# Kernel optimization log

Measured on AMD Instinct MI355X. Metric: run time of the kernel, lower is better.

Reference implementation:

```python
import jax, jax.numpy as jnp
import numpy as np

H = 256; HID = 128; V = 50000; LV = 200
N = 512; L = 64; M = 64; C = 4; T = 8; K = 8; E = 2048


def _gru_cell(x, h, wih, whh, bih, bhh):
    gi = x @ wih.T + bih
    gh = h @ whh.T + bhh
    ir, iz, inn = jnp.split(gi, 3, -1)
    hr, hz, hn = jnp.split(gh, 3, -1)
    r = jax.nn.sigmoid(ir + hr)
    z = jax.nn.sigmoid(iz + hz)
    n = jnp.tanh(inn + r * hn)
    return (1.0 - z) * n + z * h


def _bigru(x, wih, whh, bih, bhh):
    # x: [B, L, D]; params stacked [2, ...] = (fwd, bwd). out [B, L, 2*hid]
    B = x.shape[0]
    hid = whh.shape[-1]
    def run(xseq, d):
        def step(h, xt):
            hn = _gru_cell(xt, h, wih[d], whh[d], bih[d], bhh[d])
            return hn, hn
        _, out = jax.lax.scan(step, jnp.zeros((B, hid), x.dtype), jnp.swapaxes(xseq, 0, 1))
        return jnp.swapaxes(out, 0, 1)
    fwd = run(x, 0)
    bwd = jnp.flip(run(jnp.flip(x, 1), 1), 1)
    return jnp.concatenate([fwd, bwd], -1)


def _attn_pool(x, w, b):
    # x: [..., L, H]; softmax over L (matches torch softmax(dim=0) per sequence)
    a = jnp.einsum('...lh,h->...l', x, w) + b
    wts = jax.nn.softmax(a, axis=-1)
    return jnp.einsum('...l,...lh->...h', wts, x)


def _forward(seq_emb, seq_wih, seq_whh, seq_bih, seq_bhh, seq_pw, seq_pb,
             ctx_wih, ctx_whh, ctx_bih, ctx_bhh, ctx_pw, ctx_pb,
             ast_label_tab, ast_tok_tab, ast_pw, ast_pb,
             tl_wiou, tl_biou, tl_uiou, tl_wf, tl_bf, tl_uf,
             fa_wih, fa_whh, fa_bih, fa_bhh, fa_aw, fa_ab,
             comb_w, comb_b, g1_w, g1_b, g2_w, g2_b,
             cls_w1, cls_b1, cls_w2, cls_b2,
             seq_tokens, ast_children, ast_child_mask, ast_label_ids, ast_tok_ids, ctx_nei, edges):
    n_stmt = seq_tokens.shape[1]
    # --- three sequence encoders (stmt/varname/vartype), vmapped over encoder axis
    def enc(toks, emb, wih, whh, bih, bhh, pw, pb):
        e = emb[toks]                              # [N, L, H]
        o = _bigru(e, wih, whh, bih, bhh)          # [N, L, H]
        return _attn_pool(o, pw, pb)               # [N, H]
    vecs = jax.vmap(enc)(seq_tokens, seq_emb, seq_wih, seq_whh, seq_bih, seq_bhh, seq_pw, seq_pb)
    stmt_v, varn_v, vart_v = vecs[0], vecs[1], vecs[2]
    # --- ChildSum TreeLSTM over AST, batched over statements, scanned by node index
    # (children always have lower index than parent -> valid topological order)
    tok_e = ast_tok_tab[ast_tok_ids].mean(2)       # [N, M, H]
    xn = 0.5 * ast_label_tab[ast_label_ids] + 0.5 * tok_e
    Mn = xn.shape[1]
    xs = jnp.swapaxes(xn, 0, 1)                    # [M, N, H]
    chs = jnp.swapaxes(ast_children, 0, 1)         # [M, N, C]
    cms = jnp.swapaxes(ast_child_mask, 0, 1).astype(xn.dtype)
    nidx = jnp.arange(xn.shape[0])[:, None]
    def tl_step(carry, inp):
        h_arr, c_arr = carry                       # [M, N, H] each
        m, x, ch, msk = inp
        ch_h = h_arr[ch, nidx] * msk[..., None]    # [N, C, H], masked children
        ch_c = c_arr[ch, nidx] * msk[..., None]
        h_sum = ch_h.sum(1)
        iou = x @ tl_wiou.T + tl_biou + h_sum @ tl_uiou.T
        i, o, u = jnp.split(iou, 3, -1)
        i = jax.nn.sigmoid(i); o = jax.nn.sigmoid(o); u = jnp.tanh(u)
        fg = jax.nn.sigmoid((x @ tl_wf.T + tl_bf)[:, None, :] + ch_h @ tl_uf.T)
        c = i * u + (fg * ch_c).sum(1)
        h = o * jnp.tanh(c)
        return (h_arr.at[m].set(h), c_arr.at[m].set(c)), None
    z0 = jnp.zeros((Mn, xn.shape[0], xn.shape[2]), xn.dtype)
    (h_arr, _), _ = jax.lax.scan(tl_step, (z0, z0), (jnp.arange(Mn), xs, chs, cms))
    ast_v = _attn_pool(jnp.swapaxes(h_arr, 0, 1), ast_pw, ast_pb)   # [N, H]
    # --- context encoder over neighbor statement vectors (detached in original)
    ctx_in = jax.lax.stop_gradient(stmt_v)[ctx_nei]                 # [N, K, H]
    ctx_v = _attn_pool(_bigru(ctx_in, ctx_wih, ctx_whh, ctx_bih, ctx_bhh), ctx_pw, ctx_pb)
    # --- feature attention over the 5 per-statement feature vectors
    feats = jnp.stack([stmt_v, ast_v, varn_v, vart_v, ctx_v], axis=1)  # [N, 5, H]
    o = _bigru(feats, fa_wih, fa_whh, fa_bih, fa_bhh)
    wts = jax.nn.softmax(o @ fa_aw + fa_ab, axis=-1)
    x = jnp.einsum('nl,nlh->nh', wts, feats)
    # --- neighbor-mean combine (undirected unique edges)
    e0, e1 = edges[:, 0], edges[:, 1]
    rows = jnp.concatenate([e0, e1]); srcs = jnp.concatenate([e1, e0])
    nei_sum = jax.ops.segment_sum(x[srcs], rows, num_segments=n_stmt)
    deg = jax.ops.segment_sum(jnp.ones(rows.shape[0], x.dtype), rows, num_segments=n_stmt)
    nei_mean = nei_sum / jnp.maximum(deg, 1.0)[:, None]
    x2 = jax.nn.relu(jnp.concatenate([x, nei_mean], -1) @ comb_w.T + comb_b)
    # --- 2-layer symmetric-normalized GCN (edges both directions + self loops)
    sl = jnp.arange(n_stmt)
    r2 = jnp.concatenate([e0, e1, sl]); c2 = jnp.concatenate([e1, e0, sl])
    d2 = jax.ops.segment_sum(jnp.ones(r2.shape[0], x.dtype), r2, num_segments=n_stmt)
    dis = jnp.maximum(d2, 1.0) ** -0.5
    norm = (dis[r2] * dis[c2])[:, None]
    spmm = lambda y: jax.ops.segment_sum(norm * y[c2], r2, num_segments=n_stmt)
    h1 = jax.nn.relu(spmm(x2 @ g1_w.T + g1_b))
    h2 = jax.nn.relu(spmm(h1 @ g2_w.T + g2_b))
    gvec = jnp.concatenate([h2.mean(0), h2.max(0)], -1)
    return (jax.nn.relu(gvec @ cls_w1.T + cls_b1) @ cls_w2.T + cls_b2)[0]


def setup_inputs() -> dict:
    rng = np.random.default_rng(0)
    ks = iter(jax.random.split(jax.random.key(0), 64))
    def p(shape, s=0.05):
        return jax.random.normal(next(ks), shape, dtype=jnp.float32) * s
    inp = {}
    inp['seq_tokens'] = jnp.asarray(rng.integers(0, V, (3, N, L)), jnp.int32)
    ub = np.maximum(np.arange(M), 1)
    inp['ast_children'] = jnp.asarray((rng.random((N, M, C)) * ub[None, :, None]).astype(np.int64), jnp.int32)
    inp['ast_child_mask'] = jnp.asarray((rng.random((N, M, C)) < 0.7) & (np.arange(M)[None, :, None] > 0))
    inp['ast_label_ids'] = jnp.asarray(rng.integers(0, LV, (N, M)), jnp.int32)
    inp['ast_tok_ids'] = jnp.asarray(rng.integers(0, V, (N, M, T)), jnp.int32)
    inp['ctx_nei'] = jnp.asarray(rng.integers(0, N, (N, K)), jnp.int32)
    pairs = rng.integers(0, N, (8 * E, 2))
    pairs = pairs[pairs[:, 0] < pairs[:, 1]]
    pairs = np.unique(pairs, axis=0)[:E]
    inp['edges'] = jnp.asarray(pairs, jnp.int32)
    inp['seq_emb'] = p((3, V, H)).at[:, 0].set(0.0)  # padding_idx=0
    inp['seq_wih'] = p((3, 2, 3 * HID, H)); inp['seq_whh'] = p((3, 2, 3 * HID, HID))
    inp['seq_bih'] = p((3, 2, 3 * HID)); inp['seq_bhh'] = p((3, 2, 3 * HID))
    inp['seq_pw'] = p((3, H)); inp['seq_pb'] = p((3,))
    inp['ctx_wih'] = p((2, 3 * HID, H)); inp['ctx_whh'] = p((2, 3 * HID, HID))
    inp['ctx_bih'] = p((2, 3 * HID)); inp['ctx_bhh'] = p((2, 3 * HID))
    inp['ctx_pw'] = p((H,)); inp['ctx_pb'] = p(())
    inp['ast_label_tab'] = p((LV, H)); inp['ast_tok_tab'] = p((V, H))
    inp['ast_pw'] = p((H,)); inp['ast_pb'] = p(())
    inp['tl_wiou'] = p((3 * H, H)); inp['tl_biou'] = p((3 * H,)); inp['tl_uiou'] = p((3 * H, H))
    inp['tl_wf'] = p((H, H)); inp['tl_bf'] = p((H,)); inp['tl_uf'] = p((H, H))
    inp['fa_wih'] = p((2, 3 * HID, H)); inp['fa_whh'] = p((2, 3 * HID, HID))
    inp['fa_bih'] = p((2, 3 * HID)); inp['fa_bhh'] = p((2, 3 * HID))
    inp['fa_aw'] = p((H,)); inp['fa_ab'] = p(())
    inp['comb_w'] = p((H, 2 * H)); inp['comb_b'] = p((H,))
    inp['g1_w'] = p((H, H)); inp['g1_b'] = p((H,))
    inp['g2_w'] = p((H, H)); inp['g2_b'] = p((H,))
    inp['cls_w1'] = p((H, 2 * H)); inp['cls_b1'] = p((H,))
    inp['cls_w2'] = p((1, H)); inp['cls_b2'] = p((1,))
    return inp


def reference(seq_emb, seq_wih, seq_whh, seq_bih, seq_bhh, seq_pw, seq_pb,
              ctx_wih, ctx_whh, ctx_bih, ctx_bhh, ctx_pw, ctx_pb,
              ast_label_tab, ast_tok_tab, ast_pw, ast_pb,
              tl_wiou, tl_biou, tl_uiou, tl_wf, tl_bf, tl_uf,
              fa_wih, fa_whh, fa_bih, fa_bhh, fa_aw, fa_ab,
              comb_w, comb_b, g1_w, g1_b, g2_w, g2_b,
              cls_w1, cls_b1, cls_w2, cls_b2,
              seq_tokens, ast_children, ast_child_mask, ast_label_ids, ast_tok_ids, ctx_nei, edges):
    return _forward(seq_emb, seq_wih, seq_whh, seq_bih, seq_bhh, seq_pw, seq_pb,
                    ctx_wih, ctx_whh, ctx_bih, ctx_bhh, ctx_pw, ctx_pb,
                    ast_label_tab, ast_tok_tab, ast_pw, ast_pb,
                    tl_wiou, tl_biou, tl_uiou, tl_wf, tl_bf, tl_uf,
                    fa_wih, fa_whh, fa_bih, fa_bhh, fa_aw, fa_ab,
                    comb_w, comb_b, g1_w, g1_b, g2_w, g2_b,
                    cls_w1, cls_b1, cls_w2, cls_b2,
                    seq_tokens, ast_children, ast_child_mask, ast_label_ids, ast_tok_ids, ctx_nei, edges)
```

## Files before the change

### kernel.cpp

```cpp
#include <hip/hip_runtime.h>
#include <hip/hip_bf16.h>
#include <cmath>


__device__ __forceinline__ float sigf(float x) { return 1.f / (1.f + expf(-x)); }
__device__ __forceinline__ float b2f(__hip_bfloat16 x) { return __bfloat162float(x); }

typedef __attribute__((ext_vector_type(8))) short bf16x8v;
typedef __attribute__((ext_vector_type(4))) float f32x4;

__device__ __forceinline__ void gload16(const __hip_bfloat16* g, __hip_bfloat16* l) {
  __builtin_amdgcn_global_load_lds((const __attribute__((address_space(1))) void*)g,
                                   (__attribute__((address_space(3))) void*)l, 16, 0, 0);
}

__global__ __launch_bounds__(256) void k_build_wx(const float* __restrict__ wiou,
                                                  const float* __restrict__ wf,
                                                  const float* __restrict__ biou,
                                                  const float* __restrict__ bf,
                                                  float* __restrict__ w,
                                                  float* __restrict__ b) {
  int i = blockIdx.x * 256 + threadIdx.x;
  if (i < 1024 * 256) {
    int j = i >> 8, k = i & 255;
    w[i] = (j < 768) ? wiou[j * 256 + k] : wf[(j - 768) * 256 + k];
  }
  if (i < 1024) b[i] = (i < 768) ? biou[i] : bf[i - 768];
}

__global__ __launch_bounds__(256) void k_build_wproj(const float* __restrict__ uiou,
                                                     const float* __restrict__ uf,
                                                     float* __restrict__ w) {
  int i = blockIdx.x * 256 + threadIdx.x;
  if (i >= 1024 * 256) return;
  int j = i >> 8, k = i & 255;
  w[i] = (j < 768) ? uiou[j * 256 + k] : uf[(j - 768) * 256 + k];
}

__global__ __launch_bounds__(256) void k_zero_misc(float* __restrict__ nei_sum,
                                                   int* __restrict__ deg,
                                                   int* __restrict__ flag) {
  int i = blockIdx.x * 256 + threadIdx.x;
  if (i < 512 * 256) nei_sum[i] = 0.f;
  if (i < 512) deg[i] = 0;
  if (i == 0) *flag = 0;
}

__global__ __launch_bounds__(256) void k_mask_detect(const unsigned* __restrict__ raw,
                                                     int* __restrict__ flag) {
  int i = blockIdx.x * 256 + threadIdx.x;
  if (i < 32768) {
    if (raw[i] > 1u) atomicOr(flag, 1);
  }
}

__global__ __launch_bounds__(256) void k_mask_convert(const void* __restrict__ raw,
                                                      const int* __restrict__ flag,
                                                      int* __restrict__ msk) {
  int i = blockIdx.x * 256 + threadIdx.x;
  if (i >= 512 * 64 * 4) return;
  int v;
  if (*flag) v = ((const unsigned char*)raw)[i] != 0;
  else       v = ((const int*)raw)[i] != 0;
  msk[i] = v;
}

__global__ __launch_bounds__(256) void k_cvt_bf16(const float* __restrict__ A,
                                                  const int* __restrict__ ridx,
                                                  int rstride,
                                                  __hip_bfloat16* __restrict__ out) {
  int r = blockIdx.x * 8 + (threadIdx.x >> 5);
  int k = (threadIdx.x & 31) * 8;
  const float* src = A + (size_t)(ridx ? ridx[r] : r) * rstride + k;
  float4 v0 = *(const float4*)src;
  float4 v1 = *(const float4*)(src + 4);
  union { ushort4 u; __hip_bfloat16 b[4]; } p0, p1;
  p0.b[0] = __float2bfloat16(v0.x); p0.b[1] = __float2bfloat16(v0.y);
  p0.b[2] = __float2bfloat16(v0.z); p0.b[3] = __float2bfloat16(v0.w);
  p1.b[0] = __float2bfloat16(v1.x); p1.b[1] = __float2bfloat16(v1.y);
  p1.b[2] = __float2bfloat16(v1.z); p1.b[3] = __float2bfloat16(v1.w);
  __hip_bfloat16* dst = out + (size_t)r * 256 + k;
  *(ushort4*)dst = p0.u;
  *(ushort4*)(dst + 4) = p1.u;
}

__global__ __launch_bounds__(256) void k_gemm_mfma(const __hip_bfloat16* __restrict__ A,
                                                   const __hip_bfloat16* __restrict__ W,
                                                   const float* __restrict__ bias,
                                                   void* __restrict__ Cv,
                                                   int R, int K, int J,
                                                   int relu, int out_bf16) {
  __shared__ __align__(16) __hip_bfloat16 As[128 * 32];
  __shared__ __align__(16) __hip_bfloat16 Bs[128 * 32];
  int njt = J >> 7;
  int rt = blockIdx.x / njt;
  int jt = blockIdx.x - rt * njt;
  int tid = threadIdx.x;
  int w = tid >> 6, lane = tid & 63;
  int wr = w >> 1, wc = w & 1;

  const __hip_bfloat16* ga = A + (size_t)(rt * 128 + w * 32 + (lane >> 2)) * K + (lane & 3) * 8;
  const __hip_bfloat16* gb = W + (size_t)(jt * 128 + w * 32 + (lane >> 2)) * K + (lane & 3) * 8;
  __hip_bfloat16* lA0 = As + w * 1024;
  __hip_bfloat16* lB0 = Bs + w * 1024;
  size_t gstep16 = (size_t)16 * K;

  f32x4 acc[4][4];
#pragma unroll
  for (int m = 0; m < 4; ++m)
#pragma unroll
    for (int n = 0; n < 4; ++n) acc[m][n] = (f32x4){0.f, 0.f, 0.f, 0.f};

  int fr = lane & 15;
  int kg = (lane >> 4) * 8;
  const __hip_bfloat16* raA = As + (size_t)(wr * 64 + fr) * 32 + kg;
  const __hip_bfloat16* raB = Bs + (size_t)(wc * 64 + fr) * 32 + kg;

  for (int k0 = 0; k0 < K; k0 += 32) {
    __syncthreads();
    gload16(ga, lA0);
    gload16(ga + gstep16, lA0 + 512);
    gload16(gb, lB0);
    gload16(gb + gstep16, lB0 + 512);
    ga += 32; gb += 32;
    __syncthreads();
    bf16x8v a[4], b[4];
#pragma unroll
    for (int m = 0; m < 4; ++m) a[m] = *(const bf16x8v*)(raA + m * 512);
#pragma unroll
    for (int n = 0; n < 4; ++n) b[n] = *(const bf16x8v*)(raB + n * 512);
#pragma unroll
    for (int m = 0; m < 4; ++m)
#pragma unroll
      for (int n = 0; n < 4; ++n)
        acc[m][n] = __builtin_amdgcn_mfma_f32_16x16x32_bf16(a[m], b[n], acc[m][n], 0, 0, 0);
  }

  int row0 = rt * 128 + wr * 64 + (lane >> 4) * 4;
  int col0 = jt * 128 + wc * 64 + fr;
#pragma unroll
  for (int n = 0; n < 4; ++n) {
    int col = col0 + n * 16;
    float bv = bias ? bias[col] : 0.f;
#pragma unroll
    for (int m = 0; m < 4; ++m) {
#pragma unroll
      for (int j = 0; j < 4; ++j) {
        float v = acc[m][n][j] + bv;
        if (relu) v = fmaxf(v, 0.f);
        size_t idx = (size_t)(row0 + m * 16 + j) * J + col;
        if (out_bf16) ((__hip_bfloat16*)Cv)[idx] = __float2bfloat16(v);
        else ((float*)Cv)[idx] = v;
      }
    }
  }
}

__global__ __launch_bounds__(256) void k_gemm128(const float* __restrict__ A,
                                                 const int* __restrict__ ridx,
                                                 int rstride,
                                                 const float* __restrict__ W,
                                                 const float* __restrict__ bias,
                                                 float* __restrict__ C,
                                                 int R, int K, int J, int relu,
                                                 int out_bf16) {
  __shared__ float As[16][132];
  __shared__ float Ws[16][132];
  int njt = J >> 7;
  int rt = blockIdx.x / njt;
  int jt = blockIdx.x % njt;
  int tid = threadIdx.x;
  int tx = tid & 15, ty = tid >> 4;

  int row2 = tid >> 1;
  int kq = (tid & 1) * 4;
  int gr = rt * 128 + row2;
  const float* arow = A + (size_t)(ridx ? ridx[gr] : gr) * rstride;
  const float* wrow = W + (size_t)(jt * 128 + row2) * K;

  float acc[8][8];
#pragma unroll
  for (int i = 0; i < 8; ++i)
#pragma unroll
    for (int j = 0; j < 8; ++j) acc[i][j] = 0.f;

  for (int k0 = 0; k0 < K; k0 += 16) {
    float4 av0 = *(const float4*)(arow + k0 + kq);
    float4 av1 = *(const float4*)(arow + k0 + kq + 8);
    float4 wv0 = *(const float4*)(wrow + k0 + kq);
    float4 wv1 = *(const float4*)(wrow + k0 + kq + 8);
    __syncthreads();
    As[kq + 0][row2] = av0.x; As[kq + 1][row2] = av0.y;
    As[kq + 2][row2] = av0.z; As[kq + 3][row2] = av0.w;
    As[kq + 8][row2] = av1.x; As[kq + 9][row2] = av1.y;
    As[kq + 10][row2] = av1.z; As[kq + 11][row2] = av1.w;
    Ws[kq + 0][row2] = wv0.x; Ws[kq + 1][row2] = wv0.y;
    Ws[kq + 2][row2] = wv0.z; Ws[kq + 3][row2] = wv0.w;
    Ws[kq + 8][row2] = wv1.x; Ws[kq + 9][row2] = wv1.y;
    Ws[kq + 10][row2] = wv1.z; Ws[kq + 11][row2] = wv1.w;
    __syncthreads();
#pragma unroll
    for (int kk = 0; kk < 16; ++kk) {
      float a[8], b[8];
      *(float4*)&a[0] = *(const float4*)&As[kk][ty * 4];
      *(float4*)&a[4] = *(const float4*)&As[kk][64 + ty * 4];
      *(float4*)&b[0] = *(const float4*)&Ws[kk][tx * 4];
      *(float4*)&b[4] = *(const float4*)&Ws[kk][64 + tx * 4];
#pragma unroll
      for (int i = 0; i < 8; ++i)
#pragma unroll
        for (int j = 0; j < 8; ++j) acc[i][j] += a[i] * b[j];
    }
  }

  int col0 = jt * 128 + tx * 4;
  int col1 = jt * 128 + 64 + tx * 4;
  float b0[4], b1[4];
#pragma unroll
  for (int j = 0; j < 4; ++j) {
    b0[j] = bias ? bias[col0 + j] : 0.f;
    b1[j] = bias ? bias[col1 + j] : 0.f;
  }
#pragma unroll
  for (int i = 0; i < 8; ++i) {
    int row = rt * 128 + ((i < 4) ? (ty * 4 + i) : (64 + ty * 4 + i - 4));
    float v0[4], v1[4];
#pragma unroll
    for (int j = 0; j < 4; ++j) {
      float x0 = acc[i][j] + b0[j];
      float x1 = acc[i][j + 4] + b1[j];
      if (relu) { x0 = fmaxf(x0, 0.f); x1 = fmaxf(x1, 0.f); }
      v0[j] = x0; v1[j] = x1;
    }
    if (out_bf16) {
      __hip_bfloat16* Cb = (__hip_bfloat16*)C;
      union { ushort4 u; __hip_bfloat16 b[4]; } p0, p1;
#pragma unroll
      for (int j = 0; j < 4; ++j) { p0.b[j] = __float2bfloat16(v0[j]); p1.b[j] = __float2bfloat16(v1[j]); }
      *(ushort4*)(Cb + (size_t)row * J + col0) = p0.u;
      *(ushort4*)(Cb + (size_t)row * J + col1) = p1.u;
    } else {
      *(float4*)(C + (size_t)row * J + col0) = *(float4*)v0;
      *(float4*)(C + (size_t)row * J + col1) = *(float4*)v1;
    }
  }
}

__global__ __launch_bounds__(512, 2) void k_gru3(const __hip_bfloat16* __restrict__ gi,
                                                 const float* __restrict__ whh,
                                                 const float* __restrict__ bhh,
                                                 float* __restrict__ out,
                                                 int L) {
  __shared__ float hs[4][132];
  __shared__ float parts[4][8][388];
  int tid = threadIdx.x;
  int d = blockIdx.y;
  int n0 = blockIdx.x * 4;
  int ks = tid >> 6;
  int rg = tid & 63;
  int kb = ks * 16;
  const float* wbase = whh + (size_t)d * 384 * 128;

  float4 w4[6][4];
#pragma unroll
  for (int r = 0; r < 6; ++r) {
    const float* wr = wbase + (size_t)(r * 64 + rg) * 128 + kb;
#pragma unroll
    for (int q = 0; q < 4; ++q) w4[r][q] = ((const float4*)wr)[q];
  }

  int sg = tid >> 7, jg = tid & 127;
  const float* bh = bhh + d * 384;
  float br = bh[jg], bz = bh[128 + jg], bn = bh[256 + jg];

  for (int i = tid; i < 4 * 132; i += 512) ((float*)hs)[i] = 0.f;
  __syncthreads();

  int t = d ? (L - 1) : 0;
  int dt = d ? -1 : 1;

  for (int step = 0; step < L; ++step, t += dt) {
    const __hip_bfloat16* g = gi + (size_t)((n0 + sg) * L + t) * 768 + d * 384;
    float pgr = b2f(g[jg]), pgz = b2f(g[128 + jg]), pgn = b2f(g[256 + jg]);

    float acc[4][6];
#pragma unroll
    for (int s = 0; s < 4; ++s)
#pragma unroll
      for (int r = 0; r < 6; ++r) acc[s][r] = 0.f;
#pragma unroll
    for (int s = 0; s < 4; ++s) {
#pragma unroll
      for (int q = 0; q < 4; ++q) {
        float4 hv = *(const float4*)&hs[s][kb + q * 4];
#pragma unroll
        for (int r = 0; r < 6; ++r) {
          acc[s][r] += w4[r][q].x * hv.x + w4[r][q].y * hv.y +
                       w4[r][q].z * hv.z + w4[r][q].w * hv.w;
        }
      }
    }
#pragma unroll
    for (int s = 0; s < 4; ++s)
#pragma unroll
      for (int r = 0; r < 6; ++r) parts[s][ks][r * 64 + rg] = acc[s][r];
    __syncthreads();
    {
      float sr = 0.f, sz = 0.f, sn = 0.f;
#pragma unroll
      for (int k = 0; k < 8; ++k) {
        sr += parts[sg][k][jg];
        sz += parts[sg][k][128 + jg];
        sn += parts[sg][k][256 + jg];
      }
      float r = sigf(pgr + sr + br);
      float z = sigf(pgz + sz + bz);
      float nn = tanhf(pgn + r * (sn + bn));
      float hold = hs[sg][jg];
      float hnew = (1.f - z) * nn + z * hold;
      hs[sg][jg] = hnew;
      out[(size_t)((n0 + sg) * L + t) * 256 + d * 128 + jg] = hnew;
    }
    __syncthreads();
  }
}

__global__ __launch_bounds__(256) void k_attn_pool(const float* __restrict__ score_src,
                                                   int s_ns, int s_ls,
                                                   const float* __restrict__ val_src,
                                                   int v_ns, int v_ls,
                                                   const float* __restrict__ w,
                                                   const float* __restrict__ bptr,
                                                   float* __restrict__ dst,
                                                   int dst_stride, int L) {
  __shared__ float wts[64];
  int n = blockIdx.x;
  int tid = threadIdx.x;
  if (tid < 64) {
    float a = -INFINITY;
    if (tid < L) {
      const float* row = score_src + (size_t)n * s_ns + (size_t)tid * s_ls;
      float s = bptr[0];
      for (int h = 0; h < 256; h += 4) {
        float4 v = *(const float4*)(row + h);
        float4 wv = *(const float4*)(w + h);
        s += v.x * wv.x + v.y * wv.y + v.z * wv.z + v.w * wv.w;
      }
      a = s;
    }
    float mx = a;
#pragma unroll
    for (int off = 32; off; off >>= 1) mx = fmaxf(mx, __shfl_xor(mx, off));
    float e = (tid < L) ? expf(a - mx) : 0.f;
    float ss = e;
#pragma unroll
    for (int off = 32; off; off >>= 1) ss += __shfl_xor(ss, off);
    if (tid < L) wts[tid] = e / ss;
  }
  __syncthreads();
  float acc = 0.f;
  for (int l = 0; l < L; ++l)
    acc += wts[l] * val_src[(size_t)n * v_ns + (size_t)l * v_ls + tid];
  dst[(size_t)n * dst_stride + tid] = acc;
}

__global__ __launch_bounds__(256) void k_xn_bf16(const float* __restrict__ label_tab,
                                                 const float* __restrict__ tok_tab,
                                                 const int* __restrict__ lbl_ids,
                                                 const int* __restrict__ tok_ids,
                                                 __hip_bfloat16* __restrict__ xnb) {
  int nm = blockIdx.x;
  int h = threadIdx.x;
  const int* tids = tok_ids + (size_t)nm * 8;
  float s = 0.f;
#pragma unroll
  for (int t = 0; t < 8; ++t) s += tok_tab[(size_t)tids[t] * 256 + h];
  float v = 0.5f * label_tab[(size_t)lbl_ids[nm] * 256 + h] + 0.0625f * s;
  xnb[(size_t)nm * 256 + h] = __float2bfloat16(v);
}

__global__ __launch_bounds__(256) void k_tl_combine4(const __hip_bfloat16* __restrict__ HU,
                                                     const __hip_bfloat16* __restrict__ XWALL,
                                                     const int* __restrict__ ch,
                                                     const int* __restrict__ msk,
                                                     float* __restrict__ h_arr,
                                                     float* __restrict__ c_arr,
                                                     __hip_bfloat16* __restrict__ hbf,
                                                     int m) {
  int n = blockIdx.x, h = threadIdx.x;
  const __hip_bfloat16* xw = XWALL + ((size_t)(n * 64 + m)) * 1024;
  float si = b2f(xw[h]), so = b2f(xw[256 + h]), su = b2f(xw[512 + h]);
  float xfv = b2f(xw[768 + h]);
  const int* chp = ch + ((size_t)(n * 64 + m)) * 4;
  const int* mkp = msk + ((size_t)(n * 64 + m)) * 4;
  float cs = 0.f;
#pragma unroll
  for (int c = 0; c < 4; ++c) {
    if (mkp[c]) {
      int cc = chp[c];
      const __hip_bfloat16* hu = HU + ((size_t)cc * 512 + n) * 1024;
      si += b2f(hu[h]);
      so += b2f(hu[256 + h]);
      su += b2f(hu[512 + h]);
      float fg = sigf(xfv + b2f(hu[768 + h]));
      cs += fg * c_arr[((size_t)cc * 512 + n) * 256 + h];
    }
  }
  float iv = sigf(si), ov = sigf(so), uv = tanhf(su);
  float cn = iv * uv + cs;
  float hn = ov * tanhf(cn);
  h_arr[((size_t)m * 512 + n) * 256 + h] = hn;
  c_arr[((size_t)m * 512 + n) * 256 + h] = cn;
  hbf[(size_t)n * 256 + h] = __float2bfloat16(hn);
}

__global__ __launch_bounds__(256) void k_edge_deg(const int* __restrict__ edges,
                                                  int* __restrict__ deg, int E) {
  int i = blockIdx.x * 256 + threadIdx.x;
  if (i < E) {
    atomicAdd(&deg[edges[2 * i]], 1);
    atomicAdd(&deg[edges[2 * i + 1]], 1);
  }
}

__global__ __launch_bounds__(256) void k_nei(const int* __restrict__ edges,
                                             const float* __restrict__ x,
                                             float* __restrict__ nei_sum) {
  int e = blockIdx.x, h = threadIdx.x;
  int a = edges[2 * e], b = edges[2 * e + 1];
  atomicAdd(&nei_sum[(size_t)a * 256 + h], x[(size_t)b * 256 + h]);
  atomicAdd(&nei_sum[(size_t)b * 256 + h], x[(size_t)a * 256 + h]);
}

__global__ __launch_bounds__(256) void k_xcat(const float* __restrict__ x,
                                              const float* __restrict__ nei_sum,
                                              const int* __restrict__ deg,
                                              float* __restrict__ xcat) {
  int n = blockIdx.x, h = threadIdx.x;
  xcat[(size_t)n * 512 + h] = x[(size_t)n * 256 + h];
  float d = fmaxf((float)deg[n], 1.f);
  xcat[(size_t)n * 512 + 256 + h] = nei_sum[(size_t)n * 256 + h] / d;
}

__global__ __launch_bounds__(256) void k_spmm_self(const float* __restrict__ y,
                                                   const int* __restrict__ deg,
                                                   float* __restrict__ ob) {
  int n = blockIdx.x, h = threadIdx.x;
  float dis2 = 1.f / (float)(deg[n] + 1);
  ob[(size_t)n * 256 + h] = dis2 * y[(size_t)n * 256 + h];
}

__global__ __launch_bounds__(256) void k_spmm_edge(const float* __restrict__ y,
                                                   const int* __restrict__ deg,
                                                   const int* __restrict__ edges,
                                                   float* __restrict__ ob) {
  int e = blockIdx.x, h = threadIdx.x;
  int a = edges[2 * e], b = edges[2 * e + 1];
  float w = (1.f / sqrtf((float)(deg[a] + 1))) * (1.f / sqrtf((float)(deg[b] + 1)));
  atomicAdd(&ob[(size_t)a * 256 + h], w * y[(size_t)b * 256 + h]);
  atomicAdd(&ob[(size_t)b * 256 + h], w * y[(size_t)a * 256 + h]);
}

__global__ __launch_bounds__(256) void k_relu_inplace(float* __restrict__ p) {
  int i = blockIdx.x * 256 + threadIdx.x;
  p[i] = fmaxf(p[i], 0.f);
}

__global__ __launch_bounds__(256) void k_final(const float* __restrict__ h2,
                                               const float* __restrict__ w1,
                                               const float* __restrict__ b1,
                                               const float* __restrict__ w2,
                                               const float* __restrict__ b2,
                                               float* __restrict__ outp) {
  __shared__ float gv[512];
  __shared__ float zz[256];
  int tid = threadIdx.x;
  float mn = 0.f, mx = -INFINITY;
  for (int n = 0; n < 512; ++n) {
    float v = h2[(size_t)n * 256 + tid];
    mn += v;
    mx = fmaxf(mx, v);
  }
  gv[tid] = mn / 512.f;
  gv[256 + tid] = mx;
  __syncthreads();
  float acc = b1[tid];
  for (int k = 0; k < 512; ++k) acc += gv[k] * w1[(size_t)tid * 512 + k];
  zz[tid] = fmaxf(acc, 0.f) * w2[tid];
  __syncthreads();
  for (int s = 128; s; s >>= 1) {
    if (tid < s) zz[tid] += zz[tid + s];
    __syncthreads();
  }
  if (tid == 0) outp[0] = zz[0] + b2[0];
}

extern "C" void kernel_launch(void* const* d_in, const int* in_sizes, int n_in,
                              void* d_out, int out_size, void* d_ws, size_t ws_size,
                              hipStream_t stream) {
  const int* seq_tokens    = (const int*)d_in[0];
  const int* ast_children  = (const int*)d_in[1];
  const void* ast_mask_raw = (const void*)d_in[2];
  const int* ast_label_ids = (const int*)d_in[3];
  const int* ast_tok_ids   = (const int*)d_in[4];
  const int* ctx_nei       = (const int*)d_in[5];
  const int* edges         = (const int*)d_in[6];
  const float* seq_emb  = (const float*)d_in[7];
  const float* seq_wih  = (const float*)d_in[8];
  const float* seq_whh  = (const float*)d_in[9];
  const float* seq_bih  = (const float*)d_in[10];
  const float* seq_bhh  = (const float*)d_in[11];
  const float* seq_pw   = (const float*)d_in[12];
  const float* seq_pb   = (const float*)d_in[13];
  const float* ctx_wih  = (const float*)d_in[14];
  const float* ctx_whh  = (const float*)d_in[15];
  const float* ctx_bih  = (const float*)d_in[16];
  const float* ctx_bhh  = (const float*)d_in[17];
  const float* ctx_pw   = (const float*)d_in[18];
  const float* ctx_pb   = (const float*)d_in[19];
  const float* ast_label_tab = (const float*)d_in[20];
  const float* ast_tok_tab   = (const float*)d_in[21];
  const float* ast_pw   = (const float*)d_in[22];
  const float* ast_pb   = (const float*)d_in[23];
  const float* tl_wiou  = (const float*)d_in[24];
  const float* tl_biou  = (const float*)d_in[25];
  const float* tl_uiou  = (const float*)d_in[26];
  const float* tl_wf    = (const float*)d_in[27];
  const float* tl_bf    = (const float*)d_in[28];
  const float* tl_uf    = (const float*)d_in[29];
  const float* fa_wih   = (const float*)d_in[30];
  const float* fa_whh   = (const float*)d_in[31];
  const float* fa_bih   = (const float*)d_in[32];
  const float* fa_bhh   = (const float*)d_in[33];
  const float* fa_aw    = (const float*)d_in[34];
  const float* fa_ab    = (const float*)d_in[35];
  const float* comb_w   = (const float*)d_in[36];
  const float* comb_b   = (const float*)d_in[37];
  const float* g1_w     = (const float*)d_in[38];
  const float* g1_b     = (const float*)d_in[39];
  const float* g2_w     = (const float*)d_in[40];
  const float* g2_b     = (const float*)d_in[41];
  const float* cls_w1   = (const float*)d_in[42];
  const float* cls_b1   = (const float*)d_in[43];
  const float* cls_w2   = (const float*)d_in[44];
  const float* cls_b2   = (const float*)d_in[45];
  float* outp = (float*)d_out;
  float* ws = (float*)d_ws;
  int E = in_sizes[6] / 2;

  size_t off = 0;
  auto take = [&](size_t n) { size_t o = off; off += n; return o; };
  const size_t F_FEATS = take(512 * 5 * 256);
  const size_t F_X     = take(512 * 256);
  const size_t F_X2    = take(512 * 256);
  const size_t F_Y     = take(512 * 256);
  const size_t F_H1    = take(512 * 256);
  const size_t F_H2    = take(512 * 256);
  const size_t F_XCAT  = take(512 * 512);
  const size_t F_NEI   = take(512 * 256);
  const size_t F_DEG   = take(512);
  const size_t F_FLAG  = take(16);
  const size_t F_MSK   = take(512 * 64 * 4);
  const size_t F_WXW   = take(1024 * 256);
  const size_t F_WXB   = take(1024);
  const size_t F_WPROJ = take(1024 * 256);
  const size_t F_REGION = take(83886080);
  (void)ws_size;

  float* FEATS = ws + F_FEATS;
  float* X     = ws + F_X;
  float* X2    = ws + F_X2;
  float* Y     = ws + F_Y;
  float* H1    = ws + F_H1;
  float* H2    = ws + F_H2;
  float* XCAT  = ws + F_XCAT;
  float* NEI   = ws + F_NEI;
  int*   DEG   = (int*)(ws + F_DEG);
  int*   FLAG  = (int*)(ws + F_FLAG);
  int*   MSK   = (int*)(ws + F_MSK);
  float* WXW   = ws + F_WXW;
  float* WXB   = ws + F_WXB;
  float* WPROJ = ws + F_WPROJ;
  float* REG   = ws + F_REGION;
  __hip_bfloat16* GI16  = (__hip_bfloat16*)REG;
  float* OUT   = REG + 13631488;
  __hip_bfloat16* XWALL16 = (__hip_bfloat16*)REG;
  float* HARR  = REG + 17000000;
  float* CARR  = REG + 25500000;
  __hip_bfloat16* HU16 = (__hip_bfloat16*)(REG + 34000000);
  __hip_bfloat16* GIFA16 = (__hip_bfloat16*)REG;
  float* OUTFA = REG + 1966080;
  __hip_bfloat16* ABF     = (__hip_bfloat16*)(REG + 60000000);
  __hip_bfloat16* WSEQBF  = (__hip_bfloat16*)(REG + 65000000);
  __hip_bfloat16* WCTXBF  = (__hip_bfloat16*)(REG + 65400000);
  __hip_bfloat16* WFABF   = (__hip_bfloat16*)(REG + 65600000);
  __hip_bfloat16* WXWBF   = (__hip_bfloat16*)(REG + 65800000);
  __hip_bfloat16* WPROJBF = (__hip_bfloat16*)(REG + 66100000);
  __hip_bfloat16* HBF     = (__hip_bfloat16*)(REG + 66500000);

  auto gemm = [&](const float* A, const int* ridx, int rstride, const float* W,
                  const float* bias, float* C, int R, int K, int J, int relu,
                  int obf) {
    dim3 g((R / 128) * (J / 128));
    k_gemm128<<<g, 256, 0, stream>>>(A, ridx, rstride, W, bias, C, R, K, J, relu, obf);
  };
  auto cvt = [&](const float* A, const int* ridx, int rstride,
                 __hip_bfloat16* ob, int R) {
    k_cvt_bf16<<<R / 8, 256, 0, stream>>>(A, ridx, rstride, ob);
  };
  auto mgemm = [&](const __hip_bfloat16* A, const __hip_bfloat16* W,
                   const float* bias, void* C, int R, int K, int J, int relu,
                   int obf) {
    dim3 g((R / 128) * (J / 128));
    k_gemm_mfma<<<g, 256, 0, stream>>>(A, W, bias, C, R, K, J, relu, obf);
  };

  k_build_wx<<<1024, 256, 0, stream>>>(tl_wiou, tl_wf, tl_biou, tl_bf, WXW, WXB);
  k_build_wproj<<<1024, 256, 0, stream>>>(tl_uiou, tl_uf, WPROJ);
  k_zero_misc<<<512, 256, 0, stream>>>(NEI, DEG, FLAG);
  k_mask_detect<<<128, 256, 0, stream>>>((const unsigned*)ast_mask_raw, FLAG);
  k_mask_convert<<<512, 256, 0, stream>>>(ast_mask_raw, FLAG, MSK);
  cvt(seq_wih, nullptr, 256, WSEQBF, 2304);
  cvt(ctx_wih, nullptr, 256, WCTXBF, 768);
  cvt(fa_wih, nullptr, 256, WFABF, 768);
  cvt(WXW, nullptr, 256, WXWBF, 1024);
  cvt(WPROJ, nullptr, 256, WPROJBF, 1024);

  const int slot_of[3] = {0, 2, 3};
  for (int e = 0; e < 3; ++e) {
    cvt(seq_emb + (size_t)e * 50000 * 256, seq_tokens + (size_t)e * 32768, 256,
        ABF, 32768);
    mgemm(ABF, WSEQBF + (size_t)e * 768 * 256, seq_bih + (size_t)e * 768,
          GI16, 32768, 256, 768, 0, 1);
    k_gru3<<<dim3(128, 2), 512, 0, stream>>>(GI16, seq_whh + (size_t)e * 2 * 384 * 128,
                                             seq_bhh + (size_t)e * 768, OUT, 64);
    k_attn_pool<<<512, 256, 0, stream>>>(OUT, 64 * 256, 256, OUT, 64 * 256, 256,
                                         seq_pw + e * 256, seq_pb + e,
                                         FEATS + slot_of[e] * 256, 1280, 64);
  }

  cvt(FEATS, ctx_nei, 1280, ABF, 4096);
  mgemm(ABF, WCTXBF, ctx_bih, GI16, 4096, 256, 768, 0, 1);
  k_gru3<<<dim3(128, 2), 512, 0, stream>>>(GI16, ctx_whh, ctx_bhh, OUT, 8);
  k_attn_pool<<<512, 256, 0, stream>>>(OUT, 8 * 256, 256, OUT, 8 * 256, 256,
                                       ctx_pw, ctx_pb, FEATS + 4 * 256, 1280, 8);

  k_xn_bf16<<<32768, 256, 0, stream>>>(ast_label_tab, ast_tok_tab, ast_label_ids,
                                       ast_tok_ids, ABF);
  mgemm(ABF, WXWBF, WXB, XWALL16, 32768, 256, 1024, 0, 1);
  for (int m = 0; m < 64; ++m) {
    k_tl_combine4<<<512, 256, 0, stream>>>(HU16, XWALL16, ast_children, MSK,
                                           HARR, CARR, HBF, m);
    if (m < 63)
      mgemm(HBF, WPROJBF, nullptr, HU16 + (size_t)m * 512 * 1024,
            512, 256, 1024, 0, 1);
  }
  k_attn_pool<<<512, 256, 0, stream>>>(HARR, 256, 512 * 256, HARR, 256, 512 * 256,
                                       ast_pw, ast_pb, FEATS + 1 * 256, 1280, 64);

  cvt(FEATS, nullptr, 256, ABF, 2560);
  mgemm(ABF, WFABF, fa_bih, GIFA16, 2560, 256, 768, 0, 1);
  k_gru3<<<dim3(128, 2), 512, 0, stream>>>(GIFA16, fa_whh, fa_bhh, OUTFA, 5);
  k_attn_pool<<<512, 256, 0, stream>>>(OUTFA, 5 * 256, 256, FEATS, 1280, 256,
                                       fa_aw, fa_ab, X, 256, 5);

  k_edge_deg<<<(E + 255) / 256, 256, 0, stream>>>(edges, DEG, E);
  k_nei<<<E, 256, 0, stream>>>(edges, X, NEI);
  k_xcat<<<512, 256, 0, stream>>>(X, NEI, DEG, XCAT);
  gemm(XCAT, nullptr, 512, comb_w, comb_b, X2, 512, 512, 256, 1, 0);
  gemm(X2, nullptr, 256, g1_w, g1_b, Y, 512, 256, 256, 0, 0);
  k_spmm_self<<<512, 256, 0, stream>>>(Y, DEG, H1);
  k_spmm_edge<<<E, 256, 0, stream>>>(Y, DEG, edges, H1);
  k_relu_inplace<<<512, 256, 0, stream>>>(H1);
  gemm(H1, nullptr, 256, g2_w, g2_b, Y, 512, 256, 256, 0, 0);
  k_spmm_self<<<512, 256, 0, stream>>>(Y, DEG, H2);
  k_spmm_edge<<<E, 256, 0, stream>>>(Y, DEG, edges, H2);
  k_relu_inplace<<<512, 256, 0, stream>>>(H2);
  k_final<<<1, 256, 0, stream>>>(H2, cls_w1, cls_b1, cls_w2, cls_b2, outp);
}
```

Before: 2.200 ms.

## Rewrite GRU recurrence with bf16 MFMA over 16 sequences per block

Replaces the scalar-FMA GRU recurrence, which used register-held fp32 weights, 4 sequences per block and an 8-way LDS partial-sum reduction, with a kernel that issues 16x16x32 bf16 MFMA instructions over 16 sequences per block. The recurrent weights are pre-converted to bf16 and the hidden state is kept in LDS as bf16, with the gate math done 4 columns per thread. This removes the cross-warp reduction and the bulk of the scalar multiply-adds, but launches 4x fewer blocks (64 instead of 256), which may leave much of the GPU idle. It also adds bf16 rounding of the hidden state and weights on every step of the recurrence.

New measurement: 2.101 ms. 1.05x faster.

```diff
diff --git a/kernel.cpp b/kernel.cpp
--- a/kernel.cpp
+++ b/kernel.cpp
@@ -5,6 +5,9 @@
 
 __device__ __forceinline__ float sigf(float x) { return 1.f / (1.f + expf(-x)); }
 __device__ __forceinline__ float b2f(__hip_bfloat16 x) { return __bfloat162float(x); }
+__device__ __forceinline__ float bu2f(unsigned short u) {
+  union { float f; unsigned i; } v; v.i = ((unsigned)u) << 16; return v.f;
+}
 
 typedef __attribute__((ext_vector_type(8))) short bf16x8v;
 typedef __attribute__((ext_vector_type(4))) float f32x4;
@@ -246,81 +249,93 @@
   }
 }
 
-__global__ __launch_bounds__(512, 2) void k_gru3(const __hip_bfloat16* __restrict__ gi,
-                                                 const float* __restrict__ whh,
-                                                 const float* __restrict__ bhh,
-                                                 float* __restrict__ out,
-                                                 int L) {
-  __shared__ float hs[4][132];
-  __shared__ float parts[4][8][388];
+__global__ __launch_bounds__(512) void k_gru4(const __hip_bfloat16* __restrict__ gi,
+                                              const __hip_bfloat16* __restrict__ whhb,
+                                              const float* __restrict__ bhh,
+                                              float* __restrict__ out,
+                                              int L) {
+  __shared__ __align__(16) __hip_bfloat16 hsb[16][136];
+  __shared__ float outl[16][392];
   int tid = threadIdx.x;
   int d = blockIdx.y;
-  int n0 = blockIdx.x * 4;
-  int ks = tid >> 6;
-  int rg = tid & 63;
-  int kb = ks * 16;
-  const float* wbase = whh + (size_t)d * 384 * 128;
-
-  float4 w4[6][4];
-#pragma unroll
-  for (int r = 0; r < 6; ++r) {
-    const float* wr = wbase + (size_t)(r * 64 + rg) * 128 + kb;
-#pragma unroll
-    for (int q = 0; q < 4; ++q) w4[r][q] = ((const float4*)wr)[q];
-  }
-
-  int sg = tid >> 7, jg = tid & 127;
+  int n0 = blockIdx.x * 16;
+  int w = tid >> 6, lane = tid & 63;
+  int fr = lane & 15;
+  int kg = (lane >> 4) * 8;
+  int jw = w * 48;
+
+  bf16x8v bfr[3][4];
+  const __hip_bfloat16* wb = whhb + (size_t)d * 384 * 128;
+#pragma unroll
+  for (int cf = 0; cf < 3; ++cf)
+#pragma unroll
+    for (int kf = 0; kf < 4; ++kf)
+      bfr[cf][kf] = *(const bf16x8v*)(wb + (size_t)(jw + cf * 16 + fr) * 128 + kf * 32 + kg);
+
+  int s = tid >> 5;
+  int j0 = (tid & 31) * 4;
   const float* bh = bhh + d * 384;
-  float br = bh[jg], bz = bh[128 + jg], bn = bh[256 + jg];
-
-  for (int i = tid; i < 4 * 132; i += 512) ((float*)hs)[i] = 0.f;
+  float4 br = *(const float4*)(bh + j0);
+  float4 bz = *(const float4*)(bh + 128 + j0);
+  float4 bn = *(const float4*)(bh + 256 + j0);
+
+  float h[4] = {0.f, 0.f, 0.f, 0.f};
+  for (int i = tid; i < 16 * 136; i += 512) ((__hip_bfloat16*)hsb)[i] = __float2bfloat16(0.f);
   __syncthreads();
 
   int t = d ? (L - 1) : 0;
   int dt = d ? -1 : 1;
 
   for (int step = 0; step < L; ++step, t += dt) {
-    const __hip_bfloat16* g = gi + (size_t)((n0 + sg) * L + t) * 768 + d * 384;
-    float pgr = b2f(g[jg]), pgz = b2f(g[128 + jg]), pgn = b2f(g[256 + jg]);
-
-    float acc[4][6];
-#pragma unroll
-    for (int s = 0; s < 4; ++s)
-#pragma unroll
-      for (int r = 0; r < 6; ++r) acc[s][r] = 0.f;
-#pragma unroll
-    for (int s = 0; s < 4; ++s) {
-#pragma unroll
-      for (int q = 0; q < 4; ++q) {
-        float4 hv = *(const float4*)&hs[s][kb + q * 4];
-#pragma unroll
-        for (int r = 0; r < 6; ++r) {
-          acc[s][r] += w4[r][q].x * hv.x + w4[r][q].y * hv.y +
-                       w4[r][q].z * hv.z + w4[r][q].w * hv.w;
-        }
-      }
-    }
-#pragma unroll
-    for (int s = 0; s < 4; ++s)
-#pragma unroll
-      for (int r = 0; r < 6; ++r) parts[s][ks][r * 64 + rg] = acc[s][r];
+    const __hip_bfloat16* g = gi + (size_t)((n0 + s) * L + t) * 768 + d * 384 + j0;
+    ushort4 gr4 = *(const ushort4*)(g);
+    ushort4 gz4 = *(const ushort4*)(g + 128);
+    ushort4 gn4 = *(const ushort4*)(g + 256);
+
+    f32x4 acc[3];
+#pragma unroll
+    for (int cf = 0; cf < 3; ++cf) acc[cf] = (f32x4){0.f, 0.f, 0.f, 0.f};
+#pragma unroll
+    for (int kf = 0; kf < 4; ++kf) {
+      bf16x8v a = *(const bf16x8v*)(&hsb[fr][kf * 32 + kg]);
+#pragma unroll
+      for (int cf = 0; cf < 3; ++cf)
+        acc[cf] = __builtin_amdgcn_mfma_f32_16x16x32_bf16(a, bfr[cf][kf], acc[cf], 0, 0, 0);
+    }
+    int r0 = (lane >> 4) * 4;
+#pragma unroll
+    for (int cf = 0; cf < 3; ++cf) {
+      int col = jw + cf * 16 + fr;
+#pragma unroll
+      for (int r = 0; r < 4; ++r) outl[r0 + r][col] = acc[cf][r];
+    }
     __syncthreads();
-    {
-      float sr = 0.f, sz = 0.f, sn = 0.f;
-#pragma unroll
-      for (int k = 0; k < 8; ++k) {
-        sr += parts[sg][k][jg];
-        sz += parts[sg][k][128 + jg];
-        sn += parts[sg][k][256 + jg];
-      }
-      float r = sigf(pgr + sr + br);
-      float z = sigf(pgz + sz + bz);
-      float nn = tanhf(pgn + r * (sn + bn));
-      float hold = hs[sg][jg];
-      float hnew = (1.f - z) * nn + z * hold;
-      hs[sg][jg] = hnew;
-      out[(size_t)((n0 + sg) * L + t) * 256 + d * 128 + jg] = hnew;
-    }
+
+    float4 sr = *(const float4*)&outl[s][j0];
+    float4 sz = *(const float4*)&outl[s][128 + j0];
+    float4 sn = *(const float4*)&outl[s][256 + j0];
+    float gr[4] = {bu2f(gr4.x), bu2f(gr4.y), bu2f(gr4.z), bu2f(gr4.w)};
+    float gz[4] = {bu2f(gz4.x), bu2f(gz4.y), bu2f(gz4.z), bu2f(gz4.w)};
+    float gn[4] = {bu2f(gn4.x), bu2f(gn4.y), bu2f(gn4.z), bu2f(gn4.w)};
+    float srv[4] = {sr.x, sr.y, sr.z, sr.w};
+    float szv[4] = {sz.x, sz.y, sz.z, sz.w};
+    float snv[4] = {sn.x, sn.y, sn.z, sn.w};
+    float brv[4] = {br.x, br.y, br.z, br.w};
+    float bzv[4] = {bz.x, bz.y, bz.z, bz.w};
+    float bnv[4] = {bn.x, bn.y, bn.z, bn.w};
+#pragma unroll
+    for (int j = 0; j < 4; ++j) {
+      float r = sigf(gr[j] + srv[j] + brv[j]);
+      float z = sigf(gz[j] + szv[j] + bzv[j]);
+      float nn = tanhf(gn[j] + r * (snv[j] + bnv[j]));
+      h[j] = (1.f - z) * nn + z * h[j];
+    }
+    *(float4*)(out + (size_t)((n0 + s) * L + t) * 256 + d * 128 + j0) =
+        (float4){h[0], h[1], h[2], h[3]};
+    union { ushort4 u; __hip_bfloat16 b[4]; } hp;
+#pragma unroll
+    for (int j = 0; j < 4; ++j) hp.b[j] = __float2bfloat16(h[j]);
+    *(ushort4*)&hsb[s][j0] = hp.u;
     __syncthreads();
   }
 }
@@ -597,6 +612,9 @@
   __hip_bfloat16* WXWBF   = (__hip_bfloat16*)(REG + 65800000);
   __hip_bfloat16* WPROJBF = (__hip_bfloat16*)(REG + 66100000);
   __hip_bfloat16* HBF     = (__hip_bfloat16*)(REG + 66500000);
+  __hip_bfloat16* WHHSEQBF = (__hip_bfloat16*)(REG + 66600000);
+  __hip_bfloat16* WHHCTXBF = (__hip_bfloat16*)(REG + 66800000);
+  __hip_bfloat16* WHHFABF  = (__hip_bfloat16*)(REG + 66900000);
 
   auto gemm = [&](const float* A, const int* ridx, int rstride, const float* W,
                   const float* bias, float* C, int R, int K, int J, int relu,
@@ -625,6 +643,9 @@
   cvt(fa_wih, nullptr, 256, WFABF, 768);
   cvt(WXW, nullptr, 256, WXWBF, 1024);
   cvt(WPROJ, nullptr, 256, WPROJBF, 1024);
+  cvt(seq_whh, nullptr, 256, WHHSEQBF, 1152);
+  cvt(ctx_whh, nullptr, 256, WHHCTXBF, 384);
+  cvt(fa_whh, nullptr, 256, WHHFABF, 384);
 
   const int slot_of[3] = {0, 2, 3};
   for (int e = 0; e < 3; ++e) {
@@ -632,8 +653,8 @@
         ABF, 32768);
     mgemm(ABF, WSEQBF + (size_t)e * 768 * 256, seq_bih + (size_t)e * 768,
           GI16, 32768, 256, 768, 0, 1);
-    k_gru3<<<dim3(128, 2), 512, 0, stream>>>(GI16, seq_whh + (size_t)e * 2 * 384 * 128,
-                                             seq_bhh + (size_t)e * 768, OUT, 64);
+    k_gru4<<<dim3(32, 2), 512, 0, stream>>>(GI16, WHHSEQBF + (size_t)e * 2 * 384 * 128,
+                                            seq_bhh + (size_t)e * 768, OUT, 64);
     k_attn_pool<<<512, 256, 0, stream>>>(OUT, 64 * 256, 256, OUT, 64 * 256, 256,
                                          seq_pw + e * 256, seq_pb + e,
                                          FEATS + slot_of[e] * 256, 1280, 64);
@@ -641,7 +662,7 @@
 
   cvt(FEATS, ctx_nei, 1280, ABF, 4096);
   mgemm(ABF, WCTXBF, ctx_bih, GI16, 4096, 256, 768, 0, 1);
-  k_gru3<<<dim3(128, 2), 512, 0, stream>>>(GI16, ctx_whh, ctx_bhh, OUT, 8);
+  k_gru4<<<dim3(32, 2), 512, 0, stream>>>(GI16, WHHCTXBF, ctx_bhh, OUT, 8);
   k_attn_pool<<<512, 256, 0, stream>>>(OUT, 8 * 256, 256, OUT, 8 * 256, 256,
                                        ctx_pw, ctx_pb, FEATS + 4 * 256, 1280, 8);
 
@@ -660,7 +681,7 @@
 
   cvt(FEATS, nullptr, 256, ABF, 2560);
   mgemm(ABF, WFABF, fa_bih, GIFA16, 2560, 256, 768, 0, 1);
-  k_gru3<<<dim3(128, 2), 512, 0, stream>>>(GIFA16, fa_whh, fa_bhh, OUTFA, 5);
+  k_gru4<<<dim3(32, 2), 512, 0, stream>>>(GIFA16, WHHFABF, fa_bhh, OUTFA, 5);
   k_attn_pool<<<512, 256, 0, stream>>>(OUTFA, 5 * 256, 256, FEATS, 1280, 256,
                                        fa_aw, fa_ab, X, 256, 5);
 
```
